# Kernel tuning notes

Hardware: AMD Instinct MI355X
Metric: run time of the kernel (lower is better)

## Reference

```python
import jax, jax.numpy as jnp
import numpy as np

N_NODES = 100000
N_EDGES = 1600000
D_IN = 128
D_OUT = 5


def setup_inputs() -> dict:
    key = jax.random.key(0)
    k1, k2, k3, k4, k5 = jax.random.split(key, 5)
    x = jax.random.normal(k1, (N_NODES, D_IN), dtype=jnp.float32)
    edge_index = jax.random.randint(k2, (2, N_EDGES), 0, N_NODES, dtype=jnp.int64)
    scale = 1.0 / np.sqrt(D_IN)
    W_l = jax.random.normal(k3, (D_OUT, D_IN), dtype=jnp.float32) * scale
    b_l = jax.random.normal(k4, (D_OUT,), dtype=jnp.float32) * scale
    W_r = jax.random.normal(k5, (D_OUT, D_IN), dtype=jnp.float32) * scale
    return {"x": x, "edge_index": edge_index, "W_l": W_l, "b_l": b_l, "W_r": W_r}


def reference(x, edge_index, W_l, b_l, W_r):
    # PyG SAGEConv with aggr='mean', root_weight=True:
    # out_i = mean_{j: (j->i) in E} x_j @ W_l^T + b_l + x_i @ W_r^T
    n = x.shape[0]
    src = edge_index[0]
    dst = edge_index[1]
    msgs = x[src]  # [E, D_in] gather (irregular access)
    agg_sum = jax.ops.segment_sum(msgs, dst, num_segments=n)  # [N, D_in]
    deg = jax.ops.segment_sum(jnp.ones(src.shape, dtype=x.dtype), dst, num_segments=n)
    agg_mean = agg_sum / jnp.maximum(deg, 1.0)[:, None]  # zero-degree nodes -> 0
    out = agg_mean @ W_l.T + b_l + x @ W_r.T  # [N, D_out]
    return out
```

## Files before the change

### kernel.cpp

```cpp
#include <hip/hip_runtime.h>
#include <hip/hip_fp16.h>


#define N_NODES 100000
#define N_EDGES 1600000
#define D_IN 128

#define HR_STRIDE 8
#define N_PAD 100352

#define B_NODES 196
#define N_BUCKETS 512
#define CAP 3840

#define SC_EPT 8
#define SC_EPB (256 * SC_EPT)
#define SC_GRID ((N_EDGES + SC_EPB - 1) / SC_EPB)

#define NPG 8
#define PROJ_NPB (16 * NPG)
#define PROJ_BLOCKS ((N_NODES + PROJ_NPB - 1) / PROJ_NPB)
#define FUSED_GRID (PROJ_BLOCKS + SC_GRID)

#define FXS 262144.0f
#define FXB 16777216u
#define FXBF 16777216.0f
#define INV_FXS (1.0f / 262144.0f)

typedef unsigned long long u64;
typedef unsigned int u32;

__global__ __launch_bounds__(256, 4) void proj_scatter_kernel(
    const float* __restrict__ x,
    const float* __restrict__ Wl,
    const float* __restrict__ Wr,
    uint4* __restrict__ hl,
    float* __restrict__ hr,
    const int* __restrict__ ei,
    u32* __restrict__ sorted,
    int* __restrict__ cursor)
{
    const int tid = threadIdx.x;

    if (blockIdx.x < PROJ_BLOCKS) {
        const int g = tid >> 4;
        const int k = tid & 15;

        float4 wv[10][2];
#pragma unroll
        for (int o = 0; o < 10; ++o) {
            const float* w = (o < 5 ? Wl + o * D_IN : Wr + (o - 5) * D_IN) + k * 8;
            wv[o][0] = ((const float4*)w)[0];
            wv[o][1] = ((const float4*)w)[1];
        }

        const int node0 = blockIdx.x * PROJ_NPB + g * NPG;

#pragma unroll
        for (int it = 0; it < NPG; ++it) {
            const int node = min(node0 + it, N_NODES - 1);

            const float4* xr = (const float4*)(x + (size_t)node * D_IN + k * 8);
            float4 x0 = xr[0];
            float4 x1 = xr[1];

            float s[10];
#pragma unroll
            for (int o = 0; o < 10; ++o) {
                s[o] = x0.x * wv[o][0].x + x0.y * wv[o][0].y
                     + x0.z * wv[o][0].z + x0.w * wv[o][0].w
                     + x1.x * wv[o][1].x + x1.y * wv[o][1].y
                     + x1.z * wv[o][1].z + x1.w * wv[o][1].w;
            }

#pragma unroll
            for (int o = 0; o < 10; ++o) {
                s[o] += __shfl_xor(s[o], 8, 64);
                s[o] += __shfl_xor(s[o], 4, 64);
                s[o] += __shfl_xor(s[o], 2, 64);
                s[o] += __shfl_xor(s[o], 1, 64);
            }

            if (k == 0) {
                u32 u0 = (u32)__half_as_ushort(__float2half_rn(s[0]));
                u32 u1 = (u32)__half_as_ushort(__float2half_rn(s[1]));
                u32 u2 = (u32)__half_as_ushort(__float2half_rn(s[2]));
                u32 u3 = (u32)__half_as_ushort(__float2half_rn(s[3]));
                u32 u4 = (u32)__half_as_ushort(__float2half_rn(s[4]));
                uint4 pk;
                pk.x = u0 | (u1 << 16);
                pk.y = u2 | (u3 << 16);
                pk.z = u4;
                pk.w = 0u;
                hl[node] = pk;

                float* pr = hr + (size_t)node * HR_STRIDE;
                *(float4*)pr = make_float4(s[5], s[6], s[7], s[8]);
                pr[4] = s[9];
            }
        }
    } else {
        __shared__ int hist[N_BUCKETS];
        __shared__ int basepos[N_BUCKETS];

        for (int i = tid; i < N_BUCKETS; i += 256) hist[i] = 0;
        __syncthreads();

        const int blk = blockIdx.x - PROJ_BLOCKS;
        const int e0  = blk * SC_EPB + tid * SC_EPT;

        int srcv[SC_EPT], dstv[SC_EPT], slot[SC_EPT];
        bool valid[SC_EPT];

        if (e0 + SC_EPT <= N_EDGES) {
            const int4* s4 = (const int4*)(ei + e0);
            const int4* d4 = (const int4*)(ei + N_EDGES + e0);
            int4 sa = s4[0], sb = s4[1], da = d4[0], db = d4[1];
            srcv[0]=sa.x; srcv[1]=sa.y; srcv[2]=sa.z; srcv[3]=sa.w;
            srcv[4]=sb.x; srcv[5]=sb.y; srcv[6]=sb.z; srcv[7]=sb.w;
            dstv[0]=da.x; dstv[1]=da.y; dstv[2]=da.z; dstv[3]=da.w;
            dstv[4]=db.x; dstv[5]=db.y; dstv[6]=db.z; dstv[7]=db.w;
#pragma unroll
            for (int q = 0; q < SC_EPT; ++q) valid[q] = true;
        } else {
#pragma unroll
            for (int q = 0; q < SC_EPT; ++q) {
                int e = e0 + q;
                valid[q] = (e < N_EDGES);
                srcv[q] = valid[q] ? ei[e] : 0;
                dstv[q] = valid[q] ? ei[N_EDGES + e] : 0;
            }
        }

#pragma unroll
        for (int q = 0; q < SC_EPT; ++q) {
            if (valid[q]) {
                unsigned b = (unsigned)dstv[q] / 196u;
                slot[q] = atomicAdd(&hist[b], 1);
            }
        }
        __syncthreads();

        for (int b = tid; b < N_BUCKETS; b += 256) {
            int c = hist[b];
            if (c > 0) basepos[b] = atomicAdd(&cursor[b], c);
        }
        __syncthreads();

#pragma unroll
        for (int q = 0; q < SC_EPT; ++q) {
            if (valid[q]) {
                unsigned b = (unsigned)dstv[q] / 196u;
                unsigned r = (unsigned)dstv[q] - b * 196u;
                sorted[(size_t)b * CAP + basepos[b] + slot[q]] =
                    (r << 17) | (unsigned)srcv[q];
            }
        }
    }
}

__global__ __launch_bounds__(512) void agg_kernel(
    const u32* __restrict__ sorted,
    const int* __restrict__ cursor,
    const uint4* __restrict__ hl,
    const float* __restrict__ hr,
    const float* __restrict__ bias,
    float* __restrict__ out)
{
    __shared__ u64 acc[B_NODES * 3];

    const int b   = blockIdx.x;
    const int tid = threadIdx.x;

    for (int i = tid; i < B_NODES * 3; i += 512) acc[i] = 0ull;
    __syncthreads();

    const int cnt = cursor[b];
    const u32* sp = sorted + (size_t)b * CAP;
    const int nvec = cnt >> 2;

#define EMITH(hv, rr)                                                        \
    {                                                                        \
        float g0 = __half2float(__ushort_as_half((unsigned short)((hv).x & 0xFFFFu))); \
        float g1 = __half2float(__ushort_as_half((unsigned short)((hv).x >> 16)));     \
        float g2 = __half2float(__ushort_as_half((unsigned short)((hv).y & 0xFFFFu))); \
        float g3 = __half2float(__ushort_as_half((unsigned short)((hv).y >> 16)));     \
        float g4 = __half2float(__ushort_as_half((unsigned short)((hv).z & 0xFFFFu))); \
        u32 f0 = __float2uint_rn(fmaf(g0, FXS, FXBF));                       \
        u32 f1 = __float2uint_rn(fmaf(g1, FXS, FXBF));                       \
        u32 f2 = __float2uint_rn(fmaf(g2, FXS, FXBF));                       \
        u32 f3 = __float2uint_rn(fmaf(g3, FXS, FXBF));                       \
        u32 f4 = __float2uint_rn(fmaf(g4, FXS, FXBF));                       \
        u64* a = acc + (rr) * 3;                                             \
        atomicAdd(&a[0], ((u64)f1 << 32) | f0);                              \
        atomicAdd(&a[1], ((u64)f3 << 32) | f2);                              \
        atomicAdd(&a[2], ((u64)f4 << 32) | 1u);                              \
    }

    for (int it = tid; it < nvec; it += 512) {
        uint4 v = ((const uint4*)sp)[it];
        int s0 = (int)(v.x & 0x1FFFFu), r0 = (int)(v.x >> 17);
        int s1 = (int)(v.y & 0x1FFFFu), r1 = (int)(v.y >> 17);
        int s2 = (int)(v.z & 0x1FFFFu), r2 = (int)(v.z >> 17);
        int s3 = (int)(v.w & 0x1FFFFu), r3 = (int)(v.w >> 17);

        uint4 a0 = hl[s0];
        uint4 a1 = hl[s1];
        uint4 a2 = hl[s2];
        uint4 a3 = hl[s3];

        EMITH(a0, r0) EMITH(a1, r1) EMITH(a2, r2) EMITH(a3, r3)
    }
    for (int i = (nvec << 2) + tid; i < cnt; i += 512) {
        u32 v = sp[i];
        int src = (int)(v & 0x1FFFFu);
        int r   = (int)(v >> 17);
        uint4 a = hl[src];
        EMITH(a, r)
    }
#undef EMITH
    __syncthreads();

    const int nodebase = b * B_NODES;
    for (int n = tid; n < B_NODES; n += 512) {
        int node = nodebase + n;
        if (node >= N_NODES) continue;
        u64 w0 = acc[n * 3 + 0];
        u64 w1 = acc[n * 3 + 1];
        u64 w2 = acc[n * 3 + 2];
        u32 deg = (u32)(w2 & 0xFFFFFFFFu);
        u32 db  = deg * FXB;
        int i0 = (int)((u32)(w0 & 0xFFFFFFFFu) - db);
        int i1 = (int)((u32)(w0 >> 32)         - db);
        int i2 = (int)((u32)(w1 & 0xFFFFFFFFu) - db);
        int i3 = (int)((u32)(w1 >> 32)         - db);
        int i4 = (int)((u32)(w2 >> 32)         - db);

        float rec = INV_FXS / fmaxf((float)deg, 1.0f);
        const float* h = hr + (size_t)node * HR_STRIDE;
        float* o = out + (size_t)node * 5;
        o[0] = (float)i0 * rec + bias[0] + h[0];
        o[1] = (float)i1 * rec + bias[1] + h[1];
        o[2] = (float)i2 * rec + bias[2] + h[2];
        o[3] = (float)i3 * rec + bias[3] + h[3];
        o[4] = (float)i4 * rec + bias[4] + h[4];
    }
}

extern "C" void kernel_launch(void* const* d_in, const int* in_sizes, int n_in,
                              void* d_out, int out_size, void* d_ws, size_t ws_size,
                              hipStream_t stream) {
    const float* x    = (const float*)d_in[0];
    const int*   ei   = (const int*)d_in[1];
    const float* Wl   = (const float*)d_in[2];
    const float* bl   = (const float*)d_in[3];
    const float* Wr   = (const float*)d_in[4];
    float*       out  = (float*)d_out;

    uint4* hl     = (uint4*)d_ws;
    float* hr     = (float*)(hl + N_PAD);
    u32*   sorted = (u32*)(hr + (size_t)N_PAD * HR_STRIDE);
    int*   cursor = (int*)(sorted + (size_t)N_BUCKETS * CAP);

    hipMemsetAsync(cursor, 0, N_BUCKETS * sizeof(int), stream);

    proj_scatter_kernel<<<FUSED_GRID, 256, 0, stream>>>(
        x, Wl, Wr, hl, hr, ei, sorted, cursor);

    agg_kernel<<<N_BUCKETS, 512, 0, stream>>>(sorted, cursor, hl, hr, bl, out);
}
```

Before: 131.9 us.

## Interleave projection and scatter blocks, batch node loads, double edges per thread

The fused kernel now interleaves its two block roles: of every three consecutive blocks, two do projection and one does edge bucketing. Before, all projection blocks came first and all scatter blocks after. The scatter half handles 16 edges per thread instead of 8, which halves the scatter grid so it is exactly half the projection grid. The projection path loads four nodes' rows up front and then applies W_l and W_r in two separate passes, so fewer weight registers are live at once. The aim is to mix memory-bound edge traffic with projection compute on each CU and to cut register pressure. The cost is more registers per scatter thread and less parallelism in the scatter phase.

```diff
diff --git a/kernel.cpp b/kernel.cpp
--- a/kernel.cpp
+++ b/kernel.cpp
@@ -13,7 +13,7 @@
 #define N_BUCKETS 512
 #define CAP 3840
 
-#define SC_EPT 8
+#define SC_EPT 16
 #define SC_EPB (256 * SC_EPT)
 #define SC_GRID ((N_EDGES + SC_EPB - 1) / SC_EPB)
 
@@ -29,6 +29,12 @@
 
 typedef unsigned long long u64;
 typedef unsigned int u32;
+
+__device__ __forceinline__ float dot8(const float4 a0, const float4 a1,
+                                      const float4 b0, const float4 b1) {
+    return a0.x * b0.x + a0.y * b0.y + a0.z * b0.z + a0.w * b0.w
+         + a1.x * b1.x + a1.y * b1.y + a1.z * b1.z + a1.w * b1.w;
+}
 
 __global__ __launch_bounds__(256, 4) void proj_scatter_kernel(
     const float* __restrict__ x,
@@ -41,62 +47,94 @@
     int* __restrict__ cursor)
 {
     const int tid = threadIdx.x;
-
-    if (blockIdx.x < PROJ_BLOCKS) {
+    const int m   = blockIdx.x % 3;
+    const int d   = blockIdx.x / 3;
+
+    if (m < 2) {
+        const int pidx = d * 2 + m;
         const int g = tid >> 4;
         const int k = tid & 15;
-
-        float4 wv[10][2];
-#pragma unroll
-        for (int o = 0; o < 10; ++o) {
-            const float* w = (o < 5 ? Wl + o * D_IN : Wr + (o - 5) * D_IN) + k * 8;
-            wv[o][0] = ((const float4*)w)[0];
-            wv[o][1] = ((const float4*)w)[1];
-        }
-
-        const int node0 = blockIdx.x * PROJ_NPB + g * NPG;
-
-#pragma unroll
-        for (int it = 0; it < NPG; ++it) {
-            const int node = min(node0 + it, N_NODES - 1);
-
-            const float4* xr = (const float4*)(x + (size_t)node * D_IN + k * 8);
-            float4 x0 = xr[0];
-            float4 x1 = xr[1];
-
-            float s[10];
-#pragma unroll
-            for (int o = 0; o < 10; ++o) {
-                s[o] = x0.x * wv[o][0].x + x0.y * wv[o][0].y
-                     + x0.z * wv[o][0].z + x0.w * wv[o][0].w
-                     + x1.x * wv[o][1].x + x1.y * wv[o][1].y
-                     + x1.z * wv[o][1].z + x1.w * wv[o][1].w;
-            }
-
-#pragma unroll
-            for (int o = 0; o < 10; ++o) {
-                s[o] += __shfl_xor(s[o], 8, 64);
-                s[o] += __shfl_xor(s[o], 4, 64);
-                s[o] += __shfl_xor(s[o], 2, 64);
-                s[o] += __shfl_xor(s[o], 1, 64);
-            }
-
-            if (k == 0) {
-                u32 u0 = (u32)__half_as_ushort(__float2half_rn(s[0]));
-                u32 u1 = (u32)__half_as_ushort(__float2half_rn(s[1]));
-                u32 u2 = (u32)__half_as_ushort(__float2half_rn(s[2]));
-                u32 u3 = (u32)__half_as_ushort(__float2half_rn(s[3]));
-                u32 u4 = (u32)__half_as_ushort(__float2half_rn(s[4]));
-                uint4 pk;
-                pk.x = u0 | (u1 << 16);
-                pk.y = u2 | (u3 << 16);
-                pk.z = u4;
-                pk.w = 0u;
-                hl[node] = pk;
-
-                float* pr = hr + (size_t)node * HR_STRIDE;
-                *(float4*)pr = make_float4(s[5], s[6], s[7], s[8]);
-                pr[4] = s[9];
+        const int node0 = pidx * PROJ_NPB + g * NPG;
+
+#pragma unroll
+        for (int hb = 0; hb < 2; ++hb) {
+            const int nb = node0 + hb * 4;
+
+            float4 xv[4][2];
+            int nodes[4];
+#pragma unroll
+            for (int it = 0; it < 4; ++it) {
+                nodes[it] = min(nb + it, N_NODES - 1);
+                const float4* xr =
+                    (const float4*)(x + (size_t)nodes[it] * D_IN + k * 8);
+                xv[it][0] = xr[0];
+                xv[it][1] = xr[1];
+            }
+
+            {
+                float4 wv[5][2];
+#pragma unroll
+                for (int o = 0; o < 5; ++o) {
+                    const float* w = Wl + o * D_IN + k * 8;
+                    wv[o][0] = ((const float4*)w)[0];
+                    wv[o][1] = ((const float4*)w)[1];
+                }
+#pragma unroll
+                for (int it = 0; it < 4; ++it) {
+                    float s[5];
+#pragma unroll
+                    for (int o = 0; o < 5; ++o)
+                        s[o] = dot8(xv[it][0], xv[it][1], wv[o][0], wv[o][1]);
+#pragma unroll
+                    for (int o = 0; o < 5; ++o) {
+                        s[o] += __shfl_xor(s[o], 8, 64);
+                        s[o] += __shfl_xor(s[o], 4, 64);
+                        s[o] += __shfl_xor(s[o], 2, 64);
+                        s[o] += __shfl_xor(s[o], 1, 64);
+                    }
+                    if (k == 0) {
+                        u32 u0 = (u32)__half_as_ushort(__float2half_rn(s[0]));
+                        u32 u1 = (u32)__half_as_ushort(__float2half_rn(s[1]));
+                        u32 u2 = (u32)__half_as_ushort(__float2half_rn(s[2]));
+                        u32 u3 = (u32)__half_as_ushort(__float2half_rn(s[3]));
+                        u32 u4 = (u32)__half_as_ushort(__float2half_rn(s[4]));
+                        uint4 pk;
+                        pk.x = u0 | (u1 << 16);
+                        pk.y = u2 | (u3 << 16);
+                        pk.z = u4;
+                        pk.w = 0u;
+                        hl[nodes[it]] = pk;
+                    }
+                }
+            }
+
+            {
+                float4 wv[5][2];
+#pragma unroll
+                for (int o = 0; o < 5; ++o) {
+                    const float* w = Wr + o * D_IN + k * 8;
+                    wv[o][0] = ((const float4*)w)[0];
+                    wv[o][1] = ((const float4*)w)[1];
+                }
+#pragma unroll
+                for (int it = 0; it < 4; ++it) {
+                    float s[5];
+#pragma unroll
+                    for (int o = 0; o < 5; ++o)
+                        s[o] = dot8(xv[it][0], xv[it][1], wv[o][0], wv[o][1]);
+#pragma unroll
+                    for (int o = 0; o < 5; ++o) {
+                        s[o] += __shfl_xor(s[o], 8, 64);
+                        s[o] += __shfl_xor(s[o], 4, 64);
+                        s[o] += __shfl_xor(s[o], 2, 64);
+                        s[o] += __shfl_xor(s[o], 1, 64);
+                    }
+                    if (k == 0) {
+                        float* pr = hr + (size_t)nodes[it] * HR_STRIDE;
+                        *(float4*)pr = make_float4(s[0], s[1], s[2], s[3]);
+                        pr[4] = s[4];
+                    }
+                }
             }
         }
     } else {
@@ -106,8 +144,7 @@
         for (int i = tid; i < N_BUCKETS; i += 256) hist[i] = 0;
         __syncthreads();
 
-        const int blk = blockIdx.x - PROJ_BLOCKS;
-        const int e0  = blk * SC_EPB + tid * SC_EPT;
+        const int e0 = d * SC_EPB + tid * SC_EPT;
 
         int srcv[SC_EPT], dstv[SC_EPT], slot[SC_EPT];
         bool valid[SC_EPT];
@@ -115,11 +152,14 @@
         if (e0 + SC_EPT <= N_EDGES) {
             const int4* s4 = (const int4*)(ei + e0);
             const int4* d4 = (const int4*)(ei + N_EDGES + e0);
-            int4 sa = s4[0], sb = s4[1], da = d4[0], db = d4[1];
-            srcv[0]=sa.x; srcv[1]=sa.y; srcv[2]=sa.z; srcv[3]=sa.w;
-            srcv[4]=sb.x; srcv[5]=sb.y; srcv[6]=sb.z; srcv[7]=sb.w;
-            dstv[0]=da.x; dstv[1]=da.y; dstv[2]=da.z; dstv[3]=da.w;
-            dstv[4]=db.x; dstv[5]=db.y; dstv[6]=db.z; dstv[7]=db.w;
+#pragma unroll
+            for (int c = 0; c < SC_EPT / 4; ++c) {
+                int4 sv = s4[c], dv = d4[c];
+                srcv[c*4+0] = sv.x; srcv[c*4+1] = sv.y;
+                srcv[c*4+2] = sv.z; srcv[c*4+3] = sv.w;
+                dstv[c*4+0] = dv.x; dstv[c*4+1] = dv.y;
+                dstv[c*4+2] = dv.z; dstv[c*4+3] = dv.w;
+            }
 #pragma unroll
             for (int q = 0; q < SC_EPT; ++q) valid[q] = true;
         } else {
```

Result: faster. 127.7 us (-3.2%).

## Double-buffer projection x loads via global_load_lds and interleave proj/scatter blocks

Applied to the files above, without the earlier changes.

The projection branch now stages 32-node batches of x into LDS with asynchronous global_load_lds and double-buffers them, so the next batch loads while the current one is computed. Projection and scatter blocks are interleaved in a 2:1 pattern by blockIdx so both kinds of work run concurrently across the grid. Scatter blocks now process 16 edges per thread, halving their count to match the interleave. This adds LDS use, barriers and hand-written waitcnt sequencing, which may reduce occupancy or risk ordering mistakes, and the grid-size math must still match the 2:1 mapping.

```diff
diff --git a/kernel.cpp b/kernel.cpp
--- a/kernel.cpp
+++ b/kernel.cpp
@@ -13,14 +13,17 @@
 #define N_BUCKETS 512
 #define CAP 3840
 
-#define SC_EPT 8
+#define SC_EPT 16
 #define SC_EPB (256 * SC_EPT)
 #define SC_GRID ((N_EDGES + SC_EPB - 1) / SC_EPB)
 
-#define NPG 8
-#define PROJ_NPB (16 * NPG)
+#define PROJ_NPB 128
 #define PROJ_BLOCKS ((N_NODES + PROJ_NPB - 1) / PROJ_NPB)
 #define FUSED_GRID (PROJ_BLOCKS + SC_GRID)
+
+#define BB 32
+#define NBATCH (PROJ_NPB / BB)
+#define XB_BYTES (BB * 512)
 
 #define FXS 262144.0f
 #define FXB 16777216u
@@ -29,6 +32,12 @@
 
 typedef unsigned long long u64;
 typedef unsigned int u32;
+
+__device__ __forceinline__ float dot8(const float4 a0, const float4 a1,
+                                      const float4 b0, const float4 b1) {
+    return a0.x * b0.x + a0.y * b0.y + a0.z * b0.z + a0.w * b0.w
+         + a1.x * b1.x + a1.y * b1.y + a1.z * b1.z + a1.w * b1.w;
+}
 
 __global__ __launch_bounds__(256, 4) void proj_scatter_kernel(
     const float* __restrict__ x,
@@ -41,10 +50,19 @@
     int* __restrict__ cursor)
 {
     const int tid = threadIdx.x;
-
-    if (blockIdx.x < PROJ_BLOCKS) {
+    const int m   = blockIdx.x % 3;
+    const int d   = blockIdx.x / 3;
+
+    if (m < 2) {
+        __shared__ __align__(16) char xbuf[2][XB_BYTES];
+
+        const int pidx = d * 2 + m;
         const int g = tid >> 4;
         const int k = tid & 15;
+        const int node0blk = pidx * PROJ_NPB;
+
+        const char* xb = (const char*)x;
+        const size_t XLIM = (size_t)N_NODES * 512 - 16;
 
         float4 wv[10][2];
 #pragma unroll
@@ -54,51 +72,80 @@
             wv[o][1] = ((const float4*)w)[1];
         }
 
-        const int node0 = blockIdx.x * PROJ_NPB + g * NPG;
-
-#pragma unroll
-        for (int it = 0; it < NPG; ++it) {
-            const int node = min(node0 + it, N_NODES - 1);
-
-            const float4* xr = (const float4*)(x + (size_t)node * D_IN + k * 8);
-            float4 x0 = xr[0];
-            float4 x1 = xr[1];
-
-            float s[10];
-#pragma unroll
-            for (int o = 0; o < 10; ++o) {
-                s[o] = x0.x * wv[o][0].x + x0.y * wv[o][0].y
-                     + x0.z * wv[o][0].z + x0.w * wv[o][0].w
-                     + x1.x * wv[o][1].x + x1.y * wv[o][1].y
-                     + x1.z * wv[o][1].z + x1.w * wv[o][1].w;
-            }
-
-#pragma unroll
-            for (int o = 0; o < 10; ++o) {
-                s[o] += __shfl_xor(s[o], 8, 64);
-                s[o] += __shfl_xor(s[o], 4, 64);
-                s[o] += __shfl_xor(s[o], 2, 64);
-                s[o] += __shfl_xor(s[o], 1, 64);
-            }
-
-            if (k == 0) {
-                u32 u0 = (u32)__half_as_ushort(__float2half_rn(s[0]));
-                u32 u1 = (u32)__half_as_ushort(__float2half_rn(s[1]));
-                u32 u2 = (u32)__half_as_ushort(__float2half_rn(s[2]));
-                u32 u3 = (u32)__half_as_ushort(__float2half_rn(s[3]));
-                u32 u4 = (u32)__half_as_ushort(__float2half_rn(s[4]));
-                uint4 pk;
-                pk.x = u0 | (u1 << 16);
-                pk.y = u2 | (u3 << 16);
-                pk.z = u4;
-                pk.w = 0u;
-                hl[node] = pk;
-
-                float* pr = hr + (size_t)node * HR_STRIDE;
-                *(float4*)pr = make_float4(s[5], s[6], s[7], s[8]);
-                pr[4] = s[9];
-            }
-        }
+#define STAGE(bufi, batch)                                                   \
+        {                                                                    \
+            const size_t gb0 = (size_t)(node0blk + (batch) * BB) * 512;      \
+            _Pragma("unroll")                                                \
+            for (int r = 0; r < 4; ++r) {                                    \
+                const int loff = r * 4096 + tid * 16;                        \
+                size_t goff = gb0 + (size_t)loff;                            \
+                goff = goff > XLIM ? XLIM : goff;                            \
+                __builtin_amdgcn_global_load_lds(                            \
+                    (const __attribute__((address_space(1))) void*)(xb + goff), \
+                    (__attribute__((address_space(3))) void*)(&xbuf[bufi][loff]), \
+                    16, 0, 0);                                               \
+            }                                                                \
+        }
+
+        int cur = 0;
+        STAGE(0, 0);
+
+#pragma unroll
+        for (int b = 0; b < NBATCH; ++b) {
+            if (b + 1 < NBATCH) {
+                STAGE(cur ^ 1, b + 1);
+                asm volatile("s_waitcnt vmcnt(4)" ::: "memory");
+            } else {
+                asm volatile("s_waitcnt vmcnt(0)" ::: "memory");
+            }
+            __builtin_amdgcn_s_barrier();
+            asm volatile("" ::: "memory");
+
+            const char* xbc = (const char*)xbuf[cur];
+#pragma unroll
+            for (int u = 0; u < 2; ++u) {
+                const int nlb  = g * 2 + u;
+                const int node = node0blk + b * BB + nlb;
+                const float4* xp = (const float4*)(xbc + nlb * 512 + k * 32);
+                float4 x0 = xp[0];
+                float4 x1 = xp[1];
+
+                float s[10];
+#pragma unroll
+                for (int o = 0; o < 10; ++o)
+                    s[o] = dot8(x0, x1, wv[o][0], wv[o][1]);
+
+#pragma unroll
+                for (int o = 0; o < 10; ++o) {
+                    s[o] += __shfl_xor(s[o], 8, 64);
+                    s[o] += __shfl_xor(s[o], 4, 64);
+                    s[o] += __shfl_xor(s[o], 2, 64);
+                    s[o] += __shfl_xor(s[o], 1, 64);
+                }
+
+                if (k == 0) {
+                    u32 u0 = (u32)__half_as_ushort(__float2half_rn(s[0]));
+                    u32 u1 = (u32)__half_as_ushort(__float2half_rn(s[1]));
+                    u32 u2 = (u32)__half_as_ushort(__float2half_rn(s[2]));
+                    u32 u3 = (u32)__half_as_ushort(__float2half_rn(s[3]));
+                    u32 u4 = (u32)__half_as_ushort(__float2half_rn(s[4]));
+                    uint4 pk;
+                    pk.x = u0 | (u1 << 16);
+                    pk.y = u2 | (u3 << 16);
+                    pk.z = u4;
+                    pk.w = 0u;
+                    hl[node] = pk;
+
+                    float* pr = hr + (size_t)node * HR_STRIDE;
+                    *(float4*)pr = make_float4(s[5], s[6], s[7], s[8]);
+                    pr[4] = s[9];
+                }
+            }
+            __builtin_amdgcn_s_barrier();
+            asm volatile("" ::: "memory");
+            cur ^= 1;
+        }
+#undef STAGE
     } else {
         __shared__ int hist[N_BUCKETS];
         __shared__ int basepos[N_BUCKETS];
@@ -106,8 +153,7 @@
         for (int i = tid; i < N_BUCKETS; i += 256) hist[i] = 0;
         __syncthreads();
 
-        const int blk = blockIdx.x - PROJ_BLOCKS;
-        const int e0  = blk * SC_EPB + tid * SC_EPT;
+        const int e0 = d * SC_EPB + tid * SC_EPT;
 
         int srcv[SC_EPT], dstv[SC_EPT], slot[SC_EPT];
         bool valid[SC_EPT];
@@ -115,11 +161,14 @@
         if (e0 + SC_EPT <= N_EDGES) {
             const int4* s4 = (const int4*)(ei + e0);
             const int4* d4 = (const int4*)(ei + N_EDGES + e0);
-            int4 sa = s4[0], sb = s4[1], da = d4[0], db = d4[1];
-            srcv[0]=sa.x; srcv[1]=sa.y; srcv[2]=sa.z; srcv[3]=sa.w;
-            srcv[4]=sb.x; srcv[5]=sb.y; srcv[6]=sb.z; srcv[7]=sb.w;
-            dstv[0]=da.x; dstv[1]=da.y; dstv[2]=da.z; dstv[3]=da.w;
-            dstv[4]=db.x; dstv[5]=db.y; dstv[6]=db.z; dstv[7]=db.w;
+#pragma unroll
+            for (int c = 0; c < SC_EPT / 4; ++c) {
+                int4 sv = s4[c], dv = d4[c];
+                srcv[c*4+0] = sv.x; srcv[c*4+1] = sv.y;
+                srcv[c*4+2] = sv.z; srcv[c*4+3] = sv.w;
+                dstv[c*4+0] = dv.x; dstv[c*4+1] = dv.y;
+                dstv[c*4+2] = dv.z; dstv[c*4+3] = dv.w;
+            }
 #pragma unroll
             for (int q = 0; q < SC_EPT; ++q) valid[q] = true;
         } else {
```

Result: faster. 128.6 us (-2.5%).
